# Kernel optimization log

Measured on AMD Instinct MI355X. Metric: run time of the kernel, lower is better.

## Reference

```python
import jax, jax.numpy as jnp
import numpy as np

B, S, D_IN, D_OUT = 4, 2048, 1024, 1024


def setup_inputs() -> dict:
    key = jax.random.key(0)
    ks = jax.random.split(key, 6)
    scale = 1.0 / np.sqrt(D_IN)
    return {
        "inputs_for_keys": jax.random.normal(ks[0], (B, S, D_IN), jnp.float32),
        "inputs_for_values": jax.random.normal(ks[1], (B, S, D_IN), jnp.float32),
        "inputs_for_queries": jax.random.normal(ks[2], (B, S, D_IN), jnp.float32),
        "WK": jax.random.uniform(ks[3], (D_IN, D_OUT), jnp.float32, -scale, scale),
        "WQ": jax.random.uniform(ks[4], (D_IN, D_OUT), jnp.float32, -scale, scale),
        "WV": jax.random.uniform(ks[5], (D_IN, D_OUT), jnp.float32, -scale, scale),
    }


def reference(inputs_for_keys, inputs_for_values, inputs_for_queries, WK, WQ, WV):
    # QKV projections: [B,S,Din] @ [Din,Dout] -> [B,S,Dout]
    keys = jnp.einsum("bsd,de->bse", inputs_for_keys, WK)
    values = jnp.einsum("bsd,de->bse", inputs_for_values, WV)
    queries = jnp.einsum("bsd,de->bse", inputs_for_queries, WQ)
    d_k = keys.shape[-1]
    # scaled scores [B,S,S]
    scores = jnp.einsum("bqe,bke->bqk", queries, keys) / jnp.sqrt(jnp.float32(d_k))
    # causal mask: position k > q gets -inf (strictly upper triangular)
    q_idx = jnp.arange(S)[:, None]
    k_idx = jnp.arange(S)[None, :]
    scores = jnp.where(k_idx > q_idx, -jnp.inf, scores)
    att = jax.nn.softmax(scores, axis=-1)
    out = jnp.einsum("bqk,bke->bqe", att, values)  # [B,S,Dout]
    return out
```

## Files before the change

### kernel.cpp

```cpp
#include <hip/hip_runtime.h>
#include <stdint.h>


typedef __attribute__((ext_vector_type(8))) short short8;
typedef __attribute__((ext_vector_type(8))) unsigned short ushort8;
typedef __attribute__((ext_vector_type(4))) unsigned short ushort4v;
typedef __attribute__((ext_vector_type(4))) float f32x4;

__device__ __forceinline__ unsigned short f2bf(float f) {
  union { float f; unsigned u; } v; v.f = f;
  unsigned u = v.u + 0x7FFFu + ((v.u >> 16) & 1u);
  return (unsigned short)(u >> 16);
}
__device__ __forceinline__ float bf2f(unsigned short h) {
  union { unsigned u; float f; } v; v.u = ((unsigned)h) << 16;
  return v.f;
}

__device__ __forceinline__ void gload16(const void* g, void* l) {
  __builtin_amdgcn_global_load_lds(
      (const __attribute__((address_space(1))) unsigned int*)g,
      (__attribute__((address_space(3))) unsigned int*)l, 16, 0, 0);
}

template<int N> __device__ __forceinline__ void vmwait() {
  static_assert(N >= 0 && N <= 8, "vmcnt range");
  if constexpr (N == 0) asm volatile("s_waitcnt vmcnt(0)" ::: "memory");
  else if constexpr (N == 1) asm volatile("s_waitcnt vmcnt(1)" ::: "memory");
  else if constexpr (N == 2) asm volatile("s_waitcnt vmcnt(2)" ::: "memory");
  else if constexpr (N == 3) asm volatile("s_waitcnt vmcnt(3)" ::: "memory");
  else if constexpr (N == 4) asm volatile("s_waitcnt vmcnt(4)" ::: "memory");
  else if constexpr (N == 5) asm volatile("s_waitcnt vmcnt(5)" ::: "memory");
  else if constexpr (N == 6) asm volatile("s_waitcnt vmcnt(6)" ::: "memory");
  else if constexpr (N == 7) asm volatile("s_waitcnt vmcnt(7)" ::: "memory");
  else asm volatile("s_waitcnt vmcnt(8)" ::: "memory");
}
__device__ __forceinline__ void barrier_() { asm volatile("s_barrier" ::: "memory"); }
__device__ __forceinline__ void lgkm0() { asm volatile("s_waitcnt lgkmcnt(0)" ::: "memory"); }

__device__ __forceinline__ void cvt_blk(const float* __restrict__ in,
                                        unsigned short* __restrict__ out,
                                        long base, float s, int tid) {
  float4 v[8];
#pragma unroll
  for (int j = 0; j < 8; ++j)
    v[j] = *(const float4*)(in + base + j * 1024 + tid * 4);
#pragma unroll
  for (int j = 0; j < 8; ++j) {
    ushort4v r;
    r[0] = f2bf(v[j].x * s); r[1] = f2bf(v[j].y * s);
    r[2] = f2bf(v[j].z * s); r[3] = f2bf(v[j].w * s);
    *(ushort4v*)(out + base + j * 1024 + tid * 4) = r;
  }
}

__global__ __launch_bounds__(256)
void prep(const float* __restrict__ Xq, const float* __restrict__ Xk,
          const float* __restrict__ Xv,
          unsigned short* __restrict__ Oq, unsigned short* __restrict__ Ok,
          unsigned short* __restrict__ Ov,
          const float* __restrict__ WQ, const float* __restrict__ WK,
          const float* __restrict__ WV,
          unsigned short* __restrict__ WQb, unsigned short* __restrict__ WKb,
          unsigned short* __restrict__ WVT) {
  const int bx = blockIdx.x;
  const int tid = threadIdx.x;
  if (bx < 3072) {
    const int op = bx >> 10, r = bx & 1023;
    const float* in = op == 0 ? Xq : op == 1 ? Xk : Xv;
    unsigned short* out = op == 0 ? Oq : op == 1 ? Ok : Ov;
    cvt_blk(in, out, (long)r * 8192, 1.0f, tid);
  } else if (bx < 3328) {
    const int wi = bx - 3072;
    const float* in = wi < 128 ? WQ : WK;
    unsigned short* out = wi < 128 ? WQb : WKb;
    const float scale = wi < 128 ? 0.03125f : 1.0f;
    cvt_blk(in, out, (long)(wi & 127) * 8192, scale, tid);
  } else {
    const int rem = bx - 3328;
    __shared__ float tbuf[32][33];
    const int bk = (rem >> 5) * 32, be = (rem & 31) * 32;
    const int tx = tid & 31, ty = tid >> 5;
#pragma unroll
    for (int j = 0; j < 32; j += 8)
      tbuf[ty + j][tx] = WV[(long)(bk + ty + j) * 1024 + (be + tx)];
    __syncthreads();
#pragma unroll
    for (int j = 0; j < 32; j += 8)
      WVT[(long)(be + ty + j) * 1024 + (bk + tx)] = f2bf(tbuf[tx][ty + j]);
  }
}

template<typename CT, int MF, int NF>
__device__ __forceinline__ void gemm_body(const unsigned short* __restrict__ A,
                                          const unsigned short* __restrict__ B,
                                          CT* __restrict__ C,
                                          int bm, int bn, int kmax,
                                          int lda, int ldb, int ldc,
                                          char* AL, char* BL) {
  constexpr int BM = MF * 32, BN = NF * 64;
  constexpr int LA = BM / 128, LB = BN / 128;
  constexpr int S = 2 * (LA + LB);

  const int tid = threadIdx.x;
  const int lane = tid & 63, wid = tid >> 6;
  const int wr = wid >> 2, wc = wid & 3;
  const int fr = lane & 15, fq = lane >> 4;
  const int srow = tid >> 2;
  const int scol = (((tid & 3) ^ ((tid >> 3) & 3)) << 3);
  const int m0 = bm * BM, n0 = bn * BN;
  const int nt = kmax >> 6;

  f32x4 acc[MF][NF] = {};

  const unsigned short* As = A + (long)(m0 + srow) * lda + scol;
  const unsigned short* Bs = B + (long)(n0 + srow) * ldb + scol;

  auto stageTile = [&](int b, int kt) {
#pragma unroll
    for (int h = 0; h < 2; ++h) {
#pragma unroll
      for (int l = 0; l < LA; ++l)
        gload16(As + (long)l * 128 * lda + kt * 64 + h * 32,
                AL + b * (BM * 128) + h * (BM * 64) + l * 8192 + tid * 16);
#pragma unroll
      for (int l = 0; l < LB; ++l)
        gload16(Bs + (long)l * 128 * ldb + kt * 64 + h * 32,
                BL + b * (BN * 128) + h * (BN * 64) + l * 8192 + tid * 16);
    }
  };

  const int aoff = (wr * (BM / 2) + fr) * 64 + ((fq ^ ((fr >> 1) & 3)) << 4);
  const int boff = (wc * (BN / 4) + fr) * 64 + ((fq ^ ((fr >> 1) & 3)) << 4);
  auto ardf = [&](int b, int kk, int m) -> short8 {
    return *(const short8*)(AL + b * (BM * 128) + kk * (BM * 64) + aoff + m * 1024);
  };
  auto brdf = [&](int b, int kk, int n) -> short8 {
    return *(const short8*)(BL + b * (BN * 128) + kk * (BN * 64) + boff + n * 1024);
  };

  stageTile(0, 0);

  for (int u = 0; u < nt; ++u) {
    const int cb = u & 1, nb = cb ^ 1;
    lgkm0();
    barrier_();
    if (u + 1 < nt) { stageTile(nb, u + 1); vmwait<S>(); }
    else            { vmwait<0>(); }
    barrier_();
#pragma unroll
    for (int kk = 0; kk < 2; ++kk) {
      short8 bfr[NF], af[MF / 2];
#pragma unroll
      for (int n = 0; n < NF; ++n) bfr[n] = brdf(cb, kk, n);
#pragma unroll
      for (int m = 0; m < MF / 2; ++m) af[m] = ardf(cb, kk, m);
      __builtin_amdgcn_s_setprio(1);
#pragma unroll
      for (int m = 0; m < MF / 2; ++m)
#pragma unroll
        for (int n = 0; n < NF; ++n)
          acc[m][n] = __builtin_amdgcn_mfma_f32_16x16x32_bf16(af[m], bfr[n], acc[m][n], 0, 0, 0);
      __builtin_amdgcn_s_setprio(0);
#pragma unroll
      for (int m = 0; m < MF / 2; ++m) af[m] = ardf(cb, kk, MF / 2 + m);
      __builtin_amdgcn_s_setprio(1);
#pragma unroll
      for (int m = 0; m < MF / 2; ++m)
#pragma unroll
        for (int n = 0; n < NF; ++n)
          acc[MF / 2 + m][n] =
              __builtin_amdgcn_mfma_f32_16x16x32_bf16(af[m], bfr[n], acc[MF / 2 + m][n], 0, 0, 0);
      __builtin_amdgcn_s_setprio(0);
    }
  }

#pragma unroll
  for (int m = 0; m < MF; ++m) {
    const int row = m0 + wr * (BM / 2) + m * 16 + fq * 4;
#pragma unroll
    for (int n = 0; n < NF; ++n) {
      const int col = n0 + wc * (BN / 4) + n * 16 + fr;
#pragma unroll
      for (int r = 0; r < 4; ++r) {
        float v = acc[m][n][r];
        if constexpr (sizeof(CT) == 2)
          C[(long)(row + r) * ldc + col] = (CT)f2bf(v);
        else
          C[(long)(row + r) * ldc + col] = (CT)v;
      }
    }
  }
}

__global__ __launch_bounds__(512, 4)
void d2_gemm(const unsigned short* __restrict__ WVT, const unsigned short* __restrict__ Xvb,
             unsigned short* __restrict__ VT,
             const unsigned short* __restrict__ WKb, const unsigned short* __restrict__ WQb,
             unsigned short* __restrict__ Mt) {
  __shared__ __align__(16) char pool[65536];
  const int id = (blockIdx.x & 7) * 72 + (blockIdx.x >> 3);
  if (id < 512)
    gemm_body<unsigned short, 4, 2>(WVT, Xvb, VT, id >> 6, id & 63, 1024,
                                    1024, 1024, 8192, pool, pool + 32768);
  else {
    const int t = id - 512;
    gemm_body<unsigned short, 4, 2>(WKb, WQb, Mt, t >> 3, t & 7, 1024,
                                    1024, 1024, 1024, pool, pool + 32768);
  }
}

__global__ __launch_bounds__(512, 4)
void y_gemm(const unsigned short* __restrict__ Xqb, const unsigned short* __restrict__ Mt,
            unsigned short* __restrict__ Y) {
  __shared__ __align__(16) char pool[65536];
  const int id = (blockIdx.x & 7) * 64 + (blockIdx.x >> 3);
  gemm_body<unsigned short, 4, 2>(Xqb, Mt, Y, id >> 3, id & 7, 1024,
                                  1024, 1024, 1024, pool, pool + 32768);
}

__global__ __launch_bounds__(512, 4)
void scores_gemm(const unsigned short* __restrict__ Y, const unsigned short* __restrict__ Xkb,
                 unsigned short* __restrict__ S) {
  __shared__ __align__(16) char pool[65536];
  const int gid = (blockIdx.x & 7) * 68 + (blockIdx.x >> 3);
  const int bz = gid / 136, t = gid - bz * 136;
  int bm = (int)((__fsqrt_rn(8.0f * t + 1.0f) - 1.0f) * 0.5f);
  while ((bm + 1) * (bm + 2) / 2 <= t) ++bm;
  while (bm * (bm + 1) / 2 > t) --bm;
  const int bn = t - bm * (bm + 1) / 2;
  gemm_body<unsigned short, 4, 2>(Y + (long)bz * 2048 * 1024, Xkb + (long)bz * 2048 * 1024,
                                  S + (long)bz * 2048 * 2048, bm, bn, 1024,
                                  1024, 1024, 2048, pool, pool + 32768);
}

__global__ __launch_bounds__(512, 4)
void pv_gemm(const unsigned short* __restrict__ P, const unsigned short* __restrict__ VT,
             float* __restrict__ O) {
  __shared__ __align__(16) char pool[65536];
  const int b = blockIdx.x;
  int bm, r;
  if (b < 256) { bm = 15 - (b >> 5); r = b & 31; }
  else         { bm = (b - 256) >> 5; r = b & 31; }
  const int bn = r & 7, bz = r >> 3;
  gemm_body<float, 4, 2>(P + (long)bz * 2048 * 2048, VT + (long)bz * 2048,
                         O + (long)bz * 2048 * 1024, bm, bn, (bm + 1) * 128,
                         2048, 8192, 1024, pool, pool + 32768);
}

__global__ __launch_bounds__(256)
void softmax_causal(unsigned short* __restrict__ P) {
  const int row = blockIdx.x;
  const int q = row & 2047;
  unsigned short* p = P + (long)row * 2048;
  const int nfill = ((q >> 7) + 1) << 7;
  const int tid = threadIdx.x;
  const int lane = tid & 63, wid = tid >> 6;
  const int i0 = tid * 8;
  __shared__ float red[8];

  float v[8];
  float lmax = -3.0e38f;
  if (i0 <= q) {
    ushort8 v8 = *(const ushort8*)(p + i0);
#pragma unroll
    for (int j = 0; j < 8; ++j) {
      float f = bf2f(v8[j]);
      f = (i0 + j <= q) ? f : -3.0e38f;
      v[j] = f;
      lmax = fmaxf(lmax, f);
    }
  } else {
#pragma unroll
    for (int j = 0; j < 8; ++j) v[j] = -3.0e38f;
  }
#pragma unroll
  for (int off = 1; off < 64; off <<= 1)
    lmax = fmaxf(lmax, __shfl_xor(lmax, off));
  if (lane == 0) red[wid] = lmax;
  __syncthreads();
  const float mx = fmaxf(fmaxf(red[0], red[1]), fmaxf(red[2], red[3]));

  float lsum = 0.f;
#pragma unroll
  for (int j = 0; j < 8; ++j) {
    float e = __expf(v[j] - mx);
    v[j] = e;
    lsum += e;
  }
#pragma unroll
  for (int off = 1; off < 64; off <<= 1)
    lsum += __shfl_xor(lsum, off);
  if (lane == 0) red[4 + wid] = lsum;
  __syncthreads();
  const float inv = 1.0f / (red[4] + red[5] + red[6] + red[7]);

  if (i0 < nfill) {
    ushort8 r;
#pragma unroll
    for (int j = 0; j < 8; ++j)
      r[j] = (i0 + j <= q) ? f2bf(v[j] * inv) : (unsigned short)0;
    *(ushort8*)(p + i0) = r;
  }
}

extern "C" void kernel_launch(void* const* d_in, const int* in_sizes, int n_in,
                              void* d_out, int out_size, void* d_ws, size_t ws_size,
                              hipStream_t stream) {
  const float* Xk = (const float*)d_in[0];
  const float* Xv = (const float*)d_in[1];
  const float* Xq = (const float*)d_in[2];
  const float* WK = (const float*)d_in[3];
  const float* WQ = (const float*)d_in[4];
  const float* WV = (const float*)d_in[5];
  float* out = (float*)d_out;

  unsigned short* ws = (unsigned short*)d_ws;
  const long NE = 8L * 1024 * 1024;
  unsigned short* Xkb = ws + 0 * NE;
  unsigned short* Xqb = ws + 1 * NE;
  unsigned short* Xvb = ws + 2 * NE;
  unsigned short* Yb  = ws + 3 * NE;
  unsigned short* VTb = ws + 4 * NE;
  unsigned short* WQb = ws + 5 * NE;
  unsigned short* WKb = WQb + 1024 * 1024;
  unsigned short* WVT = WKb + 1024 * 1024;
  unsigned short* Mtb = WVT + 1024 * 1024;
  unsigned short* Sc  = ws + 1 * NE;

  dim3 b256(256), b512(512);
  prep<<<4352, b256, 0, stream>>>(Xq, Xk, Xv, Xqb, Xkb, Xvb,
                                  WQ, WK, WV, WQb, WKb, WVT);
  d2_gemm<<<576, b512, 0, stream>>>(WVT, Xvb, VTb, WKb, WQb, Mtb);
  y_gemm<<<512, b512, 0, stream>>>(Xqb, Mtb, Yb);
  scores_gemm<<<544, b512, 0, stream>>>(Yb, Xkb, Sc);
  softmax_causal<<<8192, b256, 0, stream>>>(Sc);
  pv_gemm<<<512, b512, 0, stream>>>(Sc, VTb, out);
}
```

Measured before the change: 148.1 us.

## Defer Xq and Xk bf16 conversion into trailing phases of downstream GEMM kernels

The prep kernel now converts only Xv and the weights. The Xq fp32-to-bf16 conversion moves to the tail of d2_gemm, and the Xk conversion moves to the tail of y_gemm, each done as a grid-stride loop after the GEMM work. This is meant to shorten the serial prep stage and hide the bandwidth-bound conversions behind compute-bound GEMM blocks. The launch bounds for those two kernels drop from 4 to 2 waves per SIMD minimum, which loosens register pressure but may reduce occupancy.

```diff
diff --git a/kernel.cpp b/kernel.cpp
--- a/kernel.cpp
+++ b/kernel.cpp
@@ -38,46 +38,60 @@
 __device__ __forceinline__ void barrier_() { asm volatile("s_barrier" ::: "memory"); }
 __device__ __forceinline__ void lgkm0() { asm volatile("s_waitcnt lgkmcnt(0)" ::: "memory"); }
 
-__device__ __forceinline__ void cvt_blk(const float* __restrict__ in,
-                                        unsigned short* __restrict__ out,
-                                        long base, float s, int tid) {
-  float4 v[8];
-#pragma unroll
-  for (int j = 0; j < 8; ++j)
-    v[j] = *(const float4*)(in + base + j * 1024 + tid * 4);
-#pragma unroll
-  for (int j = 0; j < 8; ++j) {
-    ushort4v r;
-    r[0] = f2bf(v[j].x * s); r[1] = f2bf(v[j].y * s);
-    r[2] = f2bf(v[j].z * s); r[3] = f2bf(v[j].w * s);
-    *(ushort4v*)(out + base + j * 1024 + tid * 4) = r;
+__device__ __forceinline__ void cvt_tail(const float* __restrict__ in,
+                                         unsigned short* __restrict__ out,
+                                         int bx, int nblk, int tid) {
+  for (int c = bx; c < 2048; c += nblk) {
+    const long i = (long)c * 4096 + tid * 8;
+    float4 a = *(const float4*)(in + i);
+    float4 b = *(const float4*)(in + i + 4);
+    ushort8 r;
+    r[0] = f2bf(a.x); r[1] = f2bf(a.y); r[2] = f2bf(a.z); r[3] = f2bf(a.w);
+    r[4] = f2bf(b.x); r[5] = f2bf(b.y); r[6] = f2bf(b.z); r[7] = f2bf(b.w);
+    *(ushort8*)(out + i) = r;
   }
 }
 
 __global__ __launch_bounds__(256)
-void prep(const float* __restrict__ Xq, const float* __restrict__ Xk,
-          const float* __restrict__ Xv,
-          unsigned short* __restrict__ Oq, unsigned short* __restrict__ Ok,
-          unsigned short* __restrict__ Ov,
+void prep(const float* __restrict__ Xv, unsigned short* __restrict__ Ov,
           const float* __restrict__ WQ, const float* __restrict__ WK,
           const float* __restrict__ WV,
           unsigned short* __restrict__ WQb, unsigned short* __restrict__ WKb,
           unsigned short* __restrict__ WVT) {
   const int bx = blockIdx.x;
   const int tid = threadIdx.x;
-  if (bx < 3072) {
-    const int op = bx >> 10, r = bx & 1023;
-    const float* in = op == 0 ? Xq : op == 1 ? Xk : Xv;
-    unsigned short* out = op == 0 ? Oq : op == 1 ? Ok : Ov;
-    cvt_blk(in, out, (long)r * 8192, 1.0f, tid);
-  } else if (bx < 3328) {
-    const int wi = bx - 3072;
+  if (bx < 1024) {
+    const long base = (long)bx * 8192;
+    float4 v[8];
+#pragma unroll
+    for (int j = 0; j < 8; ++j)
+      v[j] = *(const float4*)(Xv + base + j * 1024 + tid * 4);
+#pragma unroll
+    for (int j = 0; j < 8; ++j) {
+      ushort4v r;
+      r[0] = f2bf(v[j].x); r[1] = f2bf(v[j].y);
+      r[2] = f2bf(v[j].z); r[3] = f2bf(v[j].w);
+      *(ushort4v*)(Ov + base + j * 1024 + tid * 4) = r;
+    }
+  } else if (bx < 1280) {
+    const int wi = bx - 1024;
     const float* in = wi < 128 ? WQ : WK;
     unsigned short* out = wi < 128 ? WQb : WKb;
-    const float scale = wi < 128 ? 0.03125f : 1.0f;
-    cvt_blk(in, out, (long)(wi & 127) * 8192, scale, tid);
+    const float s = wi < 128 ? 0.03125f : 1.0f;
+    const long base = (long)(wi & 127) * 8192;
+    float4 v[8];
+#pragma unroll
+    for (int j = 0; j < 8; ++j)
+      v[j] = *(const float4*)(in + base + j * 1024 + tid * 4);
+#pragma unroll
+    for (int j = 0; j < 8; ++j) {
+      ushort4v r;
+      r[0] = f2bf(v[j].x * s); r[1] = f2bf(v[j].y * s);
+      r[2] = f2bf(v[j].z * s); r[3] = f2bf(v[j].w * s);
+      *(ushort4v*)(out + base + j * 1024 + tid * 4) = r;
+    }
   } else {
-    const int rem = bx - 3328;
+    const int rem = bx - 1280;
     __shared__ float tbuf[32][33];
     const int bk = (rem >> 5) * 32, be = (rem & 31) * 32;
     const int tx = tid & 31, ty = tid >> 5;
@@ -193,11 +207,12 @@
   }
 }
 
-__global__ __launch_bounds__(512, 4)
+__global__ __launch_bounds__(512, 2)
 void d2_gemm(const unsigned short* __restrict__ WVT, const unsigned short* __restrict__ Xvb,
              unsigned short* __restrict__ VT,
              const unsigned short* __restrict__ WKb, const unsigned short* __restrict__ WQb,
-             unsigned short* __restrict__ Mt) {
+             unsigned short* __restrict__ Mt,
+             const float* __restrict__ Xq, unsigned short* __restrict__ Xqb) {
   __shared__ __align__(16) char pool[65536];
   const int id = (blockIdx.x & 7) * 72 + (blockIdx.x >> 3);
   if (id < 512)
@@ -208,15 +223,18 @@
     gemm_body<unsigned short, 4, 2>(WKb, WQb, Mt, t >> 3, t & 7, 1024,
                                     1024, 1024, 1024, pool, pool + 32768);
   }
-}
-
-__global__ __launch_bounds__(512, 4)
+  cvt_tail(Xq, Xqb, blockIdx.x, 576, threadIdx.x);
+}
+
+__global__ __launch_bounds__(512, 2)
 void y_gemm(const unsigned short* __restrict__ Xqb, const unsigned short* __restrict__ Mt,
-            unsigned short* __restrict__ Y) {
+            unsigned short* __restrict__ Y,
+            const float* __restrict__ Xk, unsigned short* __restrict__ Xkb) {
   __shared__ __align__(16) char pool[65536];
   const int id = (blockIdx.x & 7) * 64 + (blockIdx.x >> 3);
   gemm_body<unsigned short, 4, 2>(Xqb, Mt, Y, id >> 3, id & 7, 1024,
                                   1024, 1024, 1024, pool, pool + 32768);
+  cvt_tail(Xk, Xkb, blockIdx.x, 512, threadIdx.x);
 }
 
 __global__ __launch_bounds__(512, 4)
@@ -329,10 +347,9 @@
   unsigned short* Sc  = ws + 1 * NE;
 
   dim3 b256(256), b512(512);
-  prep<<<4352, b256, 0, stream>>>(Xq, Xk, Xv, Xqb, Xkb, Xvb,
-                                  WQ, WK, WV, WQb, WKb, WVT);
-  d2_gemm<<<576, b512, 0, stream>>>(WVT, Xvb, VTb, WKb, WQb, Mtb);
-  y_gemm<<<512, b512, 0, stream>>>(Xqb, Mtb, Yb);
+  prep<<<2304, b256, 0, stream>>>(Xv, Xvb, WQ, WK, WV, WQb, WKb, WVT);
+  d2_gemm<<<576, b512, 0, stream>>>(WVT, Xvb, VTb, WKb, WQb, Mtb, Xq, Xqb);
+  y_gemm<<<512, b512, 0, stream>>>(Xqb, Mtb, Yb, Xk, Xkb);
   scores_gemm<<<544, b512, 0, stream>>>(Yb, Xkb, Sc);
   softmax_causal<<<8192, b256, 0, stream>>>(Sc);
   pv_gemm<<<512, b512, 0, stream>>>(Sc, VTb, out);
```

Result: no change. 146.8 us (-0.9%).
